# Kernel optimization log

Hardware: AMD Instinct MI355X
Metric: run time of the kernel (lower is better)

The kernel has to match this reference:

```python
import jax, jax.numpy as jnp
import numpy as np

M = 128      # grid length
J = 80       # number of functional features (hard-coded *80 in module)
NB = 2       # n_base (module-level global used in forward)
N = NB * J   # total tiny basis networks = 160
H = 256      # hidden width
B = 2048     # batch
LN_EPS = 1e-6


def _layernorm(z, alpha, beta):
    # torch LayerNorm variant: std is UNBIASED (torch.std default), eps added to std
    avg = z.mean(axis=-1, keepdims=True)
    std = jnp.sqrt(z.var(axis=-1, ddof=1, keepdims=True)) + LN_EPS
    return (z - avg) / std * alpha + beta


def setup_inputs() -> dict:
    key = jax.random.key(0)
    ks = jax.random.split(key, 10)
    bh = 1.0 / np.sqrt(H)  # torch Linear default init bound for fan_in=H
    u = lambda k, shp, b: jax.random.uniform(k, shp, jnp.float32, -b, b)
    return {
        "x": jax.random.normal(ks[0], (B, M, J), jnp.float32),
        "t": jnp.linspace(0.0, 1.0, M, dtype=jnp.float32),
        "W_in": u(ks[1], (N, 1, H), 1.0),        # fan_in = 1
        "b_in": u(ks[2], (N, H), 1.0),
        "W_h": u(ks[3], (3, N, H, H), bh),        # 3 hidden->hidden linears
        "b_h": u(ks[4], (3, N, H), bh),
        "W_out": u(ks[5], (N, H, 1), bh),
        "b_out": u(ks[6], (N, 1), bh),
        "ln_alpha": jax.random.normal(ks[7], (4, N, H), jnp.float32),
        "ln_beta": jax.random.normal(ks[8], (4, N, H), jnp.float32),
    }


def reference(x, t, W_in, b_in, W_h, b_h, W_out, b_out, ln_alpha, ln_beta):
    # --- evaluate all N tiny basis MLPs on the grid, batched ---
    # input layer: t (M,) x W_in (N,1,H) -> (N, M, H)
    z = jnp.einsum("m,nh->nmh", t, W_in[:, 0, :]) + b_in[:, None, :]
    z = z + _layernorm(z, ln_alpha[0][:, None, :], ln_beta[0][:, None, :])
    z = jax.nn.selu(z)  # dropout is identity in eval mode
    for i in range(3):
        z = jnp.einsum("nmh,nhk->nmk", z, W_h[i]) + b_h[i][:, None, :]
        z = z + _layernorm(z, ln_alpha[i + 1][:, None, :], ln_beta[i + 1][:, None, :])
        z = jax.nn.selu(z)
    bases = jnp.einsum("nmh,nh->nm", z, W_out[:, :, 0]) + b_out  # (N, M)

    # --- trapezoidal inner-product score ---
    h = t[1:] - t[:-1]                                   # (M-1,)
    w = jnp.zeros(M, x.dtype).at[:-1].add(h / 2).at[1:].add(h / 2)  # trapezoid weights
    bases_r = bases.reshape(J, NB, M)                    # basis i*NB+k serves feature i
    score = jnp.einsum("bmj,jkm,m->bjk", x, bases_r, w)  # (B, J, NB)
    return score.reshape(x.shape[0], J * NB)
```

## Files before the change

### kernel.cpp

```cpp
#include <hip/hip_runtime.h>
#include <math.h>

#define M_GRID 128
#define J_FEAT 80
#define NNET   160
#define HDIM   256

typedef __attribute__((ext_vector_type(8))) short v8s;
typedef __attribute__((ext_vector_type(4))) float f4;

__device__ __forceinline__ unsigned short f2bf(float f) {
    unsigned u = __float_as_uint(f);
    u += 0x7fffu + ((u >> 16) & 1u);
    return (unsigned short)(u >> 16);
}

__device__ __forceinline__ float selu_f(float x) {
    const float SC = 1.0507009873554805f;
    const float AL = 1.6732632423543772f;
    return x > 0.f ? SC * x : SC * AL * (__expf(x) - 1.f);
}

#define FENCE_BAR() do { asm volatile("s_waitcnt lgkmcnt(0)" ::: "memory"); \
                         __builtin_amdgcn_sched_barrier(0);                 \
                         __builtin_amdgcn_s_barrier(); } while (0)

__attribute__((amdgpu_flat_work_group_size(512, 512), amdgpu_waves_per_eu(2, 2)))
__global__ void basis_kernel(const float* __restrict__ t,
                             const float* __restrict__ W_in,
                             const float* __restrict__ b_in,
                             const float* __restrict__ W_h,
                             const float* __restrict__ b_h,
                             const float* __restrict__ W_out,
                             const float* __restrict__ b_out,
                             const float* __restrict__ ln_a,
                             const float* __restrict__ ln_b,
                             float* __restrict__ basesT)
{
    extern __shared__ __align__(16) unsigned char lds[];
    const int n    = blockIdx.x;
    const int tid  = threadIdx.x;
    const int l    = tid & 63;
    const int wv   = tid >> 6;
    const int lr   = l & 15;
    const int g    = l >> 4;
    const int jcol = tid & 255;
    const int o8   = tid >> 8;

    unsigned char* const actw = lds + 32768 + (size_t)wv * 8192;
    float* const P = (float*)(lds + 98304);

    float rr[2][16];
    auto issue = [&](float (&r)[16], int q) {
        const float* Wq = W_h + ((size_t)((q >> 3) * NNET + n) << 16)
                        + (size_t)((q & 7) * 32 + o8 * 16) * HDIM + jcol;
        #pragma unroll
        for (int i = 0; i < 16; ++i) r[i] = Wq[(size_t)i * HDIM];
    };
    auto convert_store = [&](float (&r)[16], int bufp) {
        #pragma unroll
        for (int o = 0; o < 2; ++o) {
            v8s pk;
            #pragma unroll
            for (int i = 0; i < 8; ++i) pk[i] = (short)f2bf(r[o * 8 + i]);
            int byte = (bufp << 14) + (o8 << 13) + jcol * 32 + (o << 4);
            byte ^= ((jcol >> 2) & 7) << 4;
            *(v8s*)(lds + byte) = pk;
        }
    };

    issue(rr[0], 0);
    issue(rr[1], 1);

    {
        const size_t nb = (size_t)n * HDIM;
        #pragma unroll
        for (int i = 0; i < 7; ++i) {
            const int idx = tid + (i << 9), grp = idx >> 8, off = idx & 255;
            float v;
            if (grp == 0)       v = W_out[nb + off];
            else if (grp < 4)   v = ln_a[((size_t)grp * NNET + n) * HDIM + off];
            else if (grp < 7)   v = ln_b[((size_t)(grp - 3) * NNET + n) * HDIM + off];
            else if (grp < 10)  v = b_h[((size_t)(grp - 7) * NNET + n) * HDIM + off];
            else if (grp == 10) v = W_in[nb + off];
            else if (grp == 11) v = b_in[nb + off];
            else if (grp == 12) v = ln_a[nb + off];
            else                v = ln_b[nb + off];
            P[idx] = v;
        }
    }
    FENCE_BAR();

    const float tval = t[wv * 16 + lr];
    {
        const float* wi = P + 2560; const float* bi = P + 2816;
        const float* la = P + 3072; const float* lb = P + 3328;
        float s_ = 0.f, q_ = 0.f;
        #pragma unroll
        for (int kt = 0; kt < 8; ++kt) {
            const int h0 = kt * 32 + g * 8;
            const f4 w0 = *(const f4*)(wi + h0), w1 = *(const f4*)(wi + h0 + 4);
            const f4 b0 = *(const f4*)(bi + h0), b1 = *(const f4*)(bi + h0 + 4);
            #pragma unroll
            for (int i = 0; i < 4; ++i) {
                float v0 = __builtin_fmaf(tval, w0[i], b0[i]);
                float v1 = __builtin_fmaf(tval, w1[i], b1[i]);
                s_ += v0 + v1; q_ += v0 * v0 + v1 * v1;
            }
        }
        s_ += __shfl_xor(s_, 16); q_ += __shfl_xor(q_, 16);
        s_ += __shfl_xor(s_, 32); q_ += __shfl_xor(q_, 32);
        const float mean = s_ * (1.f / 256.f);
        const float var  = (q_ - s_ * s_ * (1.f / 256.f)) * (1.f / 255.f);
        const float inv  = 1.f / (sqrtf(var) + 1e-6f);
        asm volatile("" ::: "memory");
        #pragma unroll
        for (int kt = 0; kt < 8; ++kt) {
            const int h0 = kt * 32 + g * 8;
            const f4 w0 = *(const f4*)(wi + h0), w1 = *(const f4*)(wi + h0 + 4);
            const f4 b0 = *(const f4*)(bi + h0), b1 = *(const f4*)(bi + h0 + 4);
            const f4 a0 = *(const f4*)(la + h0), a1 = *(const f4*)(la + h0 + 4);
            const f4 e0 = *(const f4*)(lb + h0), e1 = *(const f4*)(lb + h0 + 4);
            v8s a;
            #pragma unroll
            for (int i = 0; i < 4; ++i) {
                float v0 = __builtin_fmaf(tval, w0[i], b0[i]);
                float v1 = __builtin_fmaf(tval, w1[i], b1[i]);
                a[i]     = (short)f2bf(selu_f(v0 + (v0 - mean) * inv * a0[i] + e0[i]));
                a[i + 4] = (short)f2bf(selu_f(v1 + (v1 - mean) * inv * a1[i] + e1[i]));
            }
            *(v8s*)(actw + ((lr * 512 + h0 * 2) ^ (lr << 5))) = a;
        }
        asm volatile("s_waitcnt lgkmcnt(0)" ::: "memory");
    }

    f4 acc[16];

    #pragma unroll 1
    for (int L = 0; L < 3; ++L) {
        const f4 zero = {0.f, 0.f, 0.f, 0.f};
        #pragma unroll
        for (int ct = 0; ct < 16; ++ct) acc[ct] = zero;

        #pragma unroll
        for (int s = 0; s < 8; ++s) {
            const int q = L * 8 + s;
            convert_store(rr[s & 1], s & 1);
            if (q + 2 < 24) issue(rr[s & 1], q + 2);
            FENCE_BAR();
            const v8s af = *(const v8s*)(actw + ((lr * 512 + (s * 32 + g * 8) * 2) ^ (lr << 5)));
            #pragma unroll
            for (int ct = 0; ct < 16; ++ct) {
                const int jb = ct * 16 + lr;
                int byte = ((s & 1) << 14) + ((g >> 1) << 13) + jb * 32 + ((g & 1) << 4);
                byte ^= ((jb >> 2) & 7) << 4;
                const v8s bf = *(const v8s*)(lds + byte);
                acc[ct] = __builtin_amdgcn_mfma_f32_16x16x32_bf16(af, bf, acc[ct], 0, 0, 0);
            }
        }

        const float* bh = P + (7 + L) * 256;
        const float* la = P + (1 + L) * 256;
        const float* lb = P + (4 + L) * 256;

        float sums[4] = {0,0,0,0}, sqs[4] = {0,0,0,0};
        #pragma unroll
        for (int ct = 0; ct < 16; ++ct) {
            const float bias = bh[ct * 16 + lr];
            #pragma unroll
            for (int r = 0; r < 4; ++r) {
                float v = acc[ct][r] + bias;
                acc[ct][r] = v;
                sums[r] += v; sqs[r] += v * v;
            }
        }
        #pragma unroll
        for (int r = 0; r < 4; ++r)
            #pragma unroll
            for (int m = 1; m <= 8; m <<= 1) {
                sums[r] += __shfl_xor(sums[r], m);
                sqs[r]  += __shfl_xor(sqs[r],  m);
            }
        float mean[4], inv[4];
        #pragma unroll
        for (int r = 0; r < 4; ++r) {
            mean[r] = sums[r] * (1.f / 256.f);
            float var = (sqs[r] - sums[r] * sums[r] * (1.f / 256.f)) * (1.f / 255.f);
            inv[r] = 1.f / (sqrtf(var) + 1e-6f);
        }

        if (L < 2) {
            #pragma unroll
            for (int ct = 0; ct < 16; ++ct) {
                const float a_ = la[ct * 16 + lr], b_ = lb[ct * 16 + lr];
                #pragma unroll
                for (int r = 0; r < 4; ++r) {
                    float v  = acc[ct][r];
                    float sv = selu_f(v + (v - mean[r]) * inv[r] * a_ + b_);
                    const int row = 4 * g + r;
                    *(unsigned short*)(actw + ((row * 512 + (ct * 16 + lr) * 2) ^ (row << 5)))
                        = f2bf(sv);
                }
            }
            asm volatile("s_waitcnt lgkmcnt(0)" ::: "memory");
            __builtin_amdgcn_sched_barrier(0);
        } else {
            const float bo = b_out[n];
            float ps[4] = {0,0,0,0};
            #pragma unroll
            for (int ct = 0; ct < 16; ++ct) {
                const float a_ = la[ct * 16 + lr], b_ = lb[ct * 16 + lr];
                const float w_ = P[ct * 16 + lr];
                #pragma unroll
                for (int r = 0; r < 4; ++r) {
                    float v  = acc[ct][r];
                    float sv = selu_f(v + (v - mean[r]) * inv[r] * a_ + b_);
                    ps[r] += sv * w_;
                }
            }
            #pragma unroll
            for (int r = 0; r < 4; ++r)
                #pragma unroll
                for (int m = 1; m <= 8; m <<= 1)
                    ps[r] += __shfl_xor(ps[r], m);
            #pragma unroll
            for (int r = 0; r < 4; ++r)
                if (lr == r)
                    basesT[(size_t)(wv * 16 + 4 * g + r) * NNET + n] = ps[r] + bo;
        }
    }
}

__launch_bounds__(256)
__global__ void score_kernel(const float* __restrict__ x,
                             const float* __restrict__ t,
                             const float* __restrict__ basesT,
                             float* __restrict__ out)
{
    __shared__ float c_lds[M_GRID * 32];
    const int jt  = blockIdx.x;
    const int bt  = blockIdx.y;
    const int tid = threadIdx.x;

    for (int i = tid; i < M_GRID * 32; i += 256) {
        const int m  = i >> 5;
        const int jl = i & 31;
        const float tp = t[m == M_GRID - 1 ? M_GRID - 1 : m + 1];
        const float tm = t[m == 0 ? 0 : m - 1];
        c_lds[i] = basesT[(size_t)m * NNET + jt * 32 + jl] * 0.5f * (tp - tm);
    }
    __syncthreads();

    const int jj = tid & 31;
    const int bs = tid >> 5;
    const int jk = jt * 32 + jj;
    const int b  = bt * 8 + bs;
    const float* xp = x + (size_t)b * (M_GRID * J_FEAT) + (jk >> 1);
    float acc = 0.f;
    #pragma unroll 8
    for (int m = 0; m < M_GRID; ++m)
        acc += xp[(size_t)m * J_FEAT] * c_lds[m * 32 + jj];
    out[(size_t)b * NNET + jk] = acc;
}

extern "C" void kernel_launch(void* const* d_in, const int* in_sizes, int n_in,
                              void* d_out, int out_size, void* d_ws, size_t ws_size,
                              hipStream_t stream)
{
    const float* x     = (const float*)d_in[0];
    const float* t     = (const float*)d_in[1];
    const float* W_in  = (const float*)d_in[2];
    const float* b_in  = (const float*)d_in[3];
    const float* W_h   = (const float*)d_in[4];
    const float* b_h   = (const float*)d_in[5];
    const float* W_out = (const float*)d_in[6];
    const float* b_out = (const float*)d_in[7];
    const float* ln_a  = (const float*)d_in[8];
    const float* ln_b  = (const float*)d_in[9];
    float* basesT = (float*)d_ws;

    basis_kernel<<<dim3(NNET), dim3(512), 112640, stream>>>(
        t, W_in, b_in, W_h, b_h, W_out, b_out, ln_a, ln_b, basesT);
    score_kernel<<<dim3(5, 256), dim3(256), 0, stream>>>(
        x, t, basesT, (float*)d_out);
}
```

Before: 85.45 us.

## Specialize warps into weight-producer and MFMA-consumer groups in basis kernel

Doubles the basis kernel block to 1024 threads. Eight producer waves stream W_h slices from global memory, convert them to bf16 and store them into double-buffered LDS. Eight consumer waves only run the MFMA, layernorm and SELU epilogue, with one barrier per slice. The aim is to keep global load latency and conversion off the MFMA waves, at the cost of more threads and register pressure, and consumer waves idle while producers finish.

```diff
diff --git a/kernel.cpp b/kernel.cpp
--- a/kernel.cpp
+++ b/kernel.cpp
@@ -21,11 +21,10 @@
     return x > 0.f ? SC * x : SC * AL * (__expf(x) - 1.f);
 }
 
-#define FENCE_BAR() do { asm volatile("s_waitcnt lgkmcnt(0)" ::: "memory"); \
-                         __builtin_amdgcn_sched_barrier(0);                 \
-                         __builtin_amdgcn_s_barrier(); } while (0)
-
-__attribute__((amdgpu_flat_work_group_size(512, 512), amdgpu_waves_per_eu(2, 2)))
+#define RAW_BAR() do { __builtin_amdgcn_sched_barrier(0);                  \
+                       __builtin_amdgcn_s_barrier(); } while (0)
+
+__attribute__((amdgpu_flat_work_group_size(1024, 1024)))
 __global__ void basis_kernel(const float* __restrict__ t,
                              const float* __restrict__ W_in,
                              const float* __restrict__ b_in,
@@ -42,37 +41,37 @@
     const int tid  = threadIdx.x;
     const int l    = tid & 63;
     const int wv   = tid >> 6;
+    const bool cons = (wv < 8);
+    const int c    = wv & 7;
     const int lr   = l & 15;
     const int g    = l >> 4;
-    const int jcol = tid & 255;
-    const int o8   = tid >> 8;
-
-    unsigned char* const actw = lds + 32768 + (size_t)wv * 8192;
+    const int ptid = tid & 511;
+    const int jcol = ptid & 255;
+    const int o8   = ptid >> 8;
+
+    unsigned char* const actw = lds + 32768 + (size_t)c * 8192;
     float* const P = (float*)(lds + 98304);
 
-    float rr[2][16];
-    auto issue = [&](float (&r)[16], int q) {
+    float rr[16];
+    auto issue = [&](int q) {
         const float* Wq = W_h + ((size_t)((q >> 3) * NNET + n) << 16)
                         + (size_t)((q & 7) * 32 + o8 * 16) * HDIM + jcol;
         #pragma unroll
-        for (int i = 0; i < 16; ++i) r[i] = Wq[(size_t)i * HDIM];
+        for (int i = 0; i < 16; ++i) rr[i] = Wq[(size_t)i * HDIM];
     };
-    auto convert_store = [&](float (&r)[16], int bufp) {
+    auto convert_store = [&](int bufp) {
         #pragma unroll
         for (int o = 0; o < 2; ++o) {
             v8s pk;
             #pragma unroll
-            for (int i = 0; i < 8; ++i) pk[i] = (short)f2bf(r[o * 8 + i]);
+            for (int i = 0; i < 8; ++i) pk[i] = (short)f2bf(rr[o * 8 + i]);
             int byte = (bufp << 14) + (o8 << 13) + jcol * 32 + (o << 4);
             byte ^= ((jcol >> 2) & 7) << 4;
             *(v8s*)(lds + byte) = pk;
         }
     };
 
-    issue(rr[0], 0);
-    issue(rr[1], 1);
-
-    {
+    if (cons) {
         const size_t nb = (size_t)n * HDIM;
         #pragma unroll
         for (int i = 0; i < 7; ++i) {
@@ -88,11 +87,14 @@
             else                v = ln_b[nb + off];
             P[idx] = v;
         }
+        asm volatile("s_waitcnt lgkmcnt(0)" ::: "memory");
+    } else {
+        issue(0);
     }
-    FENCE_BAR();
-
-    const float tval = t[wv * 16 + lr];
-    {
+    RAW_BAR();
+
+    if (cons) {
+        const float tval = t[c * 16 + lr];
         const float* wi = P + 2560; const float* bi = P + 2816;
         const float* la = P + 3072; const float* lb = P + 3328;
         float s_ = 0.f, q_ = 0.f;
@@ -132,102 +134,114 @@
             *(v8s*)(actw + ((lr * 512 + h0 * 2) ^ (lr << 5))) = a;
         }
         asm volatile("s_waitcnt lgkmcnt(0)" ::: "memory");
+    } else {
+        convert_store(0);
+        asm volatile("s_waitcnt lgkmcnt(0)" ::: "memory");
+        issue(1);
     }
+    RAW_BAR();
 
     f4 acc[16];
 
     #pragma unroll 1
-    for (int L = 0; L < 3; ++L) {
-        const f4 zero = {0.f, 0.f, 0.f, 0.f};
-        #pragma unroll
-        for (int ct = 0; ct < 16; ++ct) acc[ct] = zero;
-
-        #pragma unroll
-        for (int s = 0; s < 8; ++s) {
-            const int q = L * 8 + s;
-            convert_store(rr[s & 1], s & 1);
-            if (q + 2 < 24) issue(rr[s & 1], q + 2);
-            FENCE_BAR();
+    for (int q = 0; q < 24; ++q) {
+        if (cons) {
+            const int s = q & 7, L = q >> 3;
+            if (s == 0) {
+                const f4 zero = {0.f, 0.f, 0.f, 0.f};
+                #pragma unroll
+                for (int ct = 0; ct < 16; ++ct) acc[ct] = zero;
+            }
             const v8s af = *(const v8s*)(actw + ((lr * 512 + (s * 32 + g * 8) * 2) ^ (lr << 5)));
             #pragma unroll
-            for (int ct = 0; ct < 16; ++ct) {
-                const int jb = ct * 16 + lr;
-                int byte = ((s & 1) << 14) + ((g >> 1) << 13) + jb * 32 + ((g & 1) << 4);
-                byte ^= ((jb >> 2) & 7) << 4;
-                const v8s bf = *(const v8s*)(lds + byte);
-                acc[ct] = __builtin_amdgcn_mfma_f32_16x16x32_bf16(af, bf, acc[ct], 0, 0, 0);
-            }
-        }
-
-        const float* bh = P + (7 + L) * 256;
-        const float* la = P + (1 + L) * 256;
-        const float* lb = P + (4 + L) * 256;
-
-        float sums[4] = {0,0,0,0}, sqs[4] = {0,0,0,0};
-        #pragma unroll
-        for (int ct = 0; ct < 16; ++ct) {
-            const float bias = bh[ct * 16 + lr];
-            #pragma unroll
-            for (int r = 0; r < 4; ++r) {
-                float v = acc[ct][r] + bias;
-                acc[ct][r] = v;
-                sums[r] += v; sqs[r] += v * v;
-            }
-        }
-        #pragma unroll
-        for (int r = 0; r < 4; ++r)
-            #pragma unroll
-            for (int m = 1; m <= 8; m <<= 1) {
-                sums[r] += __shfl_xor(sums[r], m);
-                sqs[r]  += __shfl_xor(sqs[r],  m);
-            }
-        float mean[4], inv[4];
-        #pragma unroll
-        for (int r = 0; r < 4; ++r) {
-            mean[r] = sums[r] * (1.f / 256.f);
-            float var = (sqs[r] - sums[r] * sums[r] * (1.f / 256.f)) * (1.f / 255.f);
-            inv[r] = 1.f / (sqrtf(var) + 1e-6f);
-        }
-
-        if (L < 2) {
-            #pragma unroll
-            for (int ct = 0; ct < 16; ++ct) {
-                const float a_ = la[ct * 16 + lr], b_ = lb[ct * 16 + lr];
+            for (int cc = 0; cc < 4; ++cc) {
+                #pragma unroll
+                for (int c4 = 0; c4 < 4; ++c4) {
+                    const int ct = cc * 4 + c4;
+                    const int jb = ct * 16 + lr;
+                    int byte = ((q & 1) << 14) + ((g >> 1) << 13) + jb * 32 + ((g & 1) << 4);
+                    byte ^= ((jb >> 2) & 7) << 4;
+                    const v8s bf = *(const v8s*)(lds + byte);
+                    acc[ct] = __builtin_amdgcn_mfma_f32_16x16x32_bf16(af, bf, acc[ct], 0, 0, 0);
+                }
+                __builtin_amdgcn_sched_barrier(0);
+            }
+            if (s == 7) {
+                const float* bh = P + (7 + L) * 256;
+                const float* la = P + (1 + L) * 256;
+                const float* lb = P + (4 + L) * 256;
+                float sums[4] = {0,0,0,0}, sqs[4] = {0,0,0,0};
+                #pragma unroll
+                for (int ct = 0; ct < 16; ++ct) {
+                    const float bias = bh[ct * 16 + lr];
+                    #pragma unroll
+                    for (int r = 0; r < 4; ++r) {
+                        float v = acc[ct][r] + bias;
+                        acc[ct][r] = v;
+                        sums[r] += v; sqs[r] += v * v;
+                    }
+                }
+                #pragma unroll
+                for (int r = 0; r < 4; ++r)
+                    #pragma unroll
+                    for (int m = 1; m <= 8; m <<= 1) {
+                        sums[r] += __shfl_xor(sums[r], m);
+                        sqs[r]  += __shfl_xor(sqs[r],  m);
+                    }
+                float mean[4], inv[4];
                 #pragma unroll
                 for (int r = 0; r < 4; ++r) {
-                    float v  = acc[ct][r];
-                    float sv = selu_f(v + (v - mean[r]) * inv[r] * a_ + b_);
-                    const int row = 4 * g + r;
-                    *(unsigned short*)(actw + ((row * 512 + (ct * 16 + lr) * 2) ^ (row << 5)))
-                        = f2bf(sv);
+                    mean[r] = sums[r] * (1.f / 256.f);
+                    float var = (sqs[r] - sums[r] * sums[r] * (1.f / 256.f)) * (1.f / 255.f);
+                    inv[r] = 1.f / (sqrtf(var) + 1e-6f);
                 }
-            }
-            asm volatile("s_waitcnt lgkmcnt(0)" ::: "memory");
-            __builtin_amdgcn_sched_barrier(0);
+                if (L < 2) {
+                    #pragma unroll
+                    for (int ct = 0; ct < 16; ++ct) {
+                        const float a_ = la[ct * 16 + lr], b_ = lb[ct * 16 + lr];
+                        #pragma unroll
+                        for (int r = 0; r < 4; ++r) {
+                            float v  = acc[ct][r];
+                            float sv = selu_f(v + (v - mean[r]) * inv[r] * a_ + b_);
+                            const int row = 4 * g + r;
+                            *(unsigned short*)(actw + ((row * 512 + (ct * 16 + lr) * 2) ^ (row << 5)))
+                                = f2bf(sv);
+                        }
+                    }
+                    asm volatile("s_waitcnt lgkmcnt(0)" ::: "memory");
+                } else {
+                    const float bo = b_out[n];
+                    float ps[4] = {0,0,0,0};
+                    #pragma unroll
+                    for (int ct = 0; ct < 16; ++ct) {
+                        const float a_ = la[ct * 16 + lr], b_ = lb[ct * 16 + lr];
+                        const float w_ = P[ct * 16 + lr];
+                        #pragma unroll
+                        for (int r = 0; r < 4; ++r) {
+                            float v  = acc[ct][r];
+                            float sv = selu_f(v + (v - mean[r]) * inv[r] * a_ + b_);
+                            ps[r] += sv * w_;
+                        }
+                    }
+                    #pragma unroll
+                    for (int r = 0; r < 4; ++r)
+                        #pragma unroll
+                        for (int m = 1; m <= 8; m <<= 1)
+                            ps[r] += __shfl_xor(ps[r], m);
+                    #pragma unroll
+                    for (int r = 0; r < 4; ++r)
+                        if (lr == r)
+                            basesT[(size_t)(c * 16 + 4 * g + r) * NNET + n] = ps[r] + bo;
+                }
+            }
         } else {
-            const float bo = b_out[n];
-            float ps[4] = {0,0,0,0};
-            #pragma unroll
-            for (int ct = 0; ct < 16; ++ct) {
-                const float a_ = la[ct * 16 + lr], b_ = lb[ct * 16 + lr];
-                const float w_ = P[ct * 16 + lr];
-                #pragma unroll
-                for (int r = 0; r < 4; ++r) {
-                    float v  = acc[ct][r];
-                    float sv = selu_f(v + (v - mean[r]) * inv[r] * a_ + b_);
-                    ps[r] += sv * w_;
-                }
-            }
-            #pragma unroll
-            for (int r = 0; r < 4; ++r)
-                #pragma unroll
-                for (int m = 1; m <= 8; m <<= 1)
-                    ps[r] += __shfl_xor(ps[r], m);
-            #pragma unroll
-            for (int r = 0; r < 4; ++r)
-                if (lr == r)
-                    basesT[(size_t)(wv * 16 + 4 * g + r) * NNET + n] = ps[r] + bo;
-        }
+            if (q + 1 < 24) {
+                convert_store((q + 1) & 1);
+                asm volatile("s_waitcnt lgkmcnt(0)" ::: "memory");
+                if (q + 2 < 24) issue(q + 2);
+            }
+        }
+        RAW_BAR();
     }
 }
 
@@ -279,7 +293,7 @@
     const float* ln_b  = (const float*)d_in[9];
     float* basesT = (float*)d_ws;
 
-    basis_kernel<<<dim3(NNET), dim3(512), 112640, stream>>>(
+    basis_kernel<<<dim3(NNET), dim3(1024), 112640, stream>>>(
         t, W_in, b_in, W_h, b_h, W_out, b_out, ln_a, ln_b, basesT);
     score_kernel<<<dim3(5, 256), dim3(256), 0, stream>>>(
         x, t, basesT, (float*)d_out);
```

Result: slower. 277.4 us (+224.6%).

## Halve basis block to 4 waves, each computing 32 rows with overlapped weight staging

Applied to the files above, without the earlier changes.

Shrinks the basis kernel from 512 to 256 threads, so each wave now handles two 16-row tiles. Each B fragment read from LDS feeds two MFMAs, which halves LDS traffic per MFMA. The weight pipeline is restructured so the bf16 conversion and store of the next K-slice, plus its global prefetch, are interleaved with the MFMAs of the current slice, with one barrier per slice. This costs more registers (two 32-float prefetch buffers and two accumulator sets) and fewer waves to hide latency.

```diff
diff --git a/kernel.cpp b/kernel.cpp
--- a/kernel.cpp
+++ b/kernel.cpp
@@ -25,7 +25,7 @@
                          __builtin_amdgcn_sched_barrier(0);                 \
                          __builtin_amdgcn_s_barrier(); } while (0)
 
-__attribute__((amdgpu_flat_work_group_size(512, 512), amdgpu_waves_per_eu(2, 2)))
+__attribute__((amdgpu_flat_work_group_size(256, 256), amdgpu_waves_per_eu(1, 1)))
 __global__ void basis_kernel(const float* __restrict__ t,
                              const float* __restrict__ W_in,
                              const float* __restrict__ b_in,
@@ -44,189 +44,232 @@
     const int wv   = tid >> 6;
     const int lr   = l & 15;
     const int g    = l >> 4;
-    const int jcol = tid & 255;
-    const int o8   = tid >> 8;
-
-    unsigned char* const actw = lds + 32768 + (size_t)wv * 8192;
+    const int jcol = tid;
+
+    unsigned char* const actw = lds + 32768 + (size_t)wv * 16384;
     float* const P = (float*)(lds + 98304);
 
-    float rr[2][16];
-    auto issue = [&](float (&r)[16], int q) {
+    float rrA[32], rrB[32];
+    auto issueA = [&](int q) {
         const float* Wq = W_h + ((size_t)((q >> 3) * NNET + n) << 16)
-                        + (size_t)((q & 7) * 32 + o8 * 16) * HDIM + jcol;
-        #pragma unroll
-        for (int i = 0; i < 16; ++i) r[i] = Wq[(size_t)i * HDIM];
-    };
-    auto convert_store = [&](float (&r)[16], int bufp) {
-        #pragma unroll
-        for (int o = 0; o < 2; ++o) {
+                        + (size_t)((q & 7) * 32) * HDIM + jcol;
+        #pragma unroll
+        for (int i = 0; i < 32; ++i) rrA[i] = Wq[(size_t)i * HDIM];
+    };
+    auto issueB = [&](int q) {
+        const float* Wq = W_h + ((size_t)((q >> 3) * NNET + n) << 16)
+                        + (size_t)((q & 7) * 32) * HDIM + jcol;
+        #pragma unroll
+        for (int i = 0; i < 32; ++i) rrB[i] = Wq[(size_t)i * HDIM];
+    };
+    auto convA = [&](int bufp) {
+        #pragma unroll
+        for (int o = 0; o < 4; ++o) {
             v8s pk;
             #pragma unroll
-            for (int i = 0; i < 8; ++i) pk[i] = (short)f2bf(r[o * 8 + i]);
-            int byte = (bufp << 14) + (o8 << 13) + jcol * 32 + (o << 4);
+            for (int i = 0; i < 8; ++i) pk[i] = (short)f2bf(rrA[o * 8 + i]);
+            int byte = (bufp << 14) + ((o >> 1) << 13) + jcol * 32 + ((o & 1) << 4);
             byte ^= ((jcol >> 2) & 7) << 4;
             *(v8s*)(lds + byte) = pk;
         }
     };
-
-    issue(rr[0], 0);
-    issue(rr[1], 1);
+    auto convB = [&](int bufp) {
+        #pragma unroll
+        for (int o = 0; o < 4; ++o) {
+            v8s pk;
+            #pragma unroll
+            for (int i = 0; i < 8; ++i) pk[i] = (short)f2bf(rrB[o * 8 + i]);
+            int byte = (bufp << 14) + ((o >> 1) << 13) + jcol * 32 + ((o & 1) << 4);
+            byte ^= ((jcol >> 2) & 7) << 4;
+            *(v8s*)(lds + byte) = pk;
+        }
+    };
+
+    issueA(0);
+    issueB(1);
 
     {
         const size_t nb = (size_t)n * HDIM;
         #pragma unroll
-        for (int i = 0; i < 7; ++i) {
-            const int idx = tid + (i << 9), grp = idx >> 8, off = idx & 255;
+        for (int grp = 0; grp < 14; ++grp) {
             float v;
-            if (grp == 0)       v = W_out[nb + off];
-            else if (grp < 4)   v = ln_a[((size_t)grp * NNET + n) * HDIM + off];
-            else if (grp < 7)   v = ln_b[((size_t)(grp - 3) * NNET + n) * HDIM + off];
-            else if (grp < 10)  v = b_h[((size_t)(grp - 7) * NNET + n) * HDIM + off];
-            else if (grp == 10) v = W_in[nb + off];
-            else if (grp == 11) v = b_in[nb + off];
-            else if (grp == 12) v = ln_a[nb + off];
-            else                v = ln_b[nb + off];
-            P[idx] = v;
+            if (grp == 0)       v = W_out[nb + tid];
+            else if (grp < 4)   v = ln_a[((size_t)grp * NNET + n) * HDIM + tid];
+            else if (grp < 7)   v = ln_b[((size_t)(grp - 3) * NNET + n) * HDIM + tid];
+            else if (grp < 10)  v = b_h[((size_t)(grp - 7) * NNET + n) * HDIM + tid];
+            else if (grp == 10) v = W_in[nb + tid];
+            else if (grp == 11) v = b_in[nb + tid];
+            else if (grp == 12) v = ln_a[nb + tid];
+            else                v = ln_b[nb + tid];
+            P[grp * 256 + tid] = v;
         }
     }
     FENCE_BAR();
 
-    const float tval = t[wv * 16 + lr];
     {
         const float* wi = P + 2560; const float* bi = P + 2816;
         const float* la = P + 3072; const float* lb = P + 3328;
-        float s_ = 0.f, q_ = 0.f;
-        #pragma unroll
-        for (int kt = 0; kt < 8; ++kt) {
-            const int h0 = kt * 32 + g * 8;
-            const f4 w0 = *(const f4*)(wi + h0), w1 = *(const f4*)(wi + h0 + 4);
-            const f4 b0 = *(const f4*)(bi + h0), b1 = *(const f4*)(bi + h0 + 4);
-            #pragma unroll
-            for (int i = 0; i < 4; ++i) {
-                float v0 = __builtin_fmaf(tval, w0[i], b0[i]);
-                float v1 = __builtin_fmaf(tval, w1[i], b1[i]);
-                s_ += v0 + v1; q_ += v0 * v0 + v1 * v1;
-            }
-        }
-        s_ += __shfl_xor(s_, 16); q_ += __shfl_xor(q_, 16);
-        s_ += __shfl_xor(s_, 32); q_ += __shfl_xor(q_, 32);
-        const float mean = s_ * (1.f / 256.f);
-        const float var  = (q_ - s_ * s_ * (1.f / 256.f)) * (1.f / 255.f);
-        const float inv  = 1.f / (sqrtf(var) + 1e-6f);
-        asm volatile("" ::: "memory");
-        #pragma unroll
-        for (int kt = 0; kt < 8; ++kt) {
-            const int h0 = kt * 32 + g * 8;
-            const f4 w0 = *(const f4*)(wi + h0), w1 = *(const f4*)(wi + h0 + 4);
-            const f4 b0 = *(const f4*)(bi + h0), b1 = *(const f4*)(bi + h0 + 4);
-            const f4 a0 = *(const f4*)(la + h0), a1 = *(const f4*)(la + h0 + 4);
-            const f4 e0 = *(const f4*)(lb + h0), e1 = *(const f4*)(lb + h0 + 4);
-            v8s a;
-            #pragma unroll
-            for (int i = 0; i < 4; ++i) {
-                float v0 = __builtin_fmaf(tval, w0[i], b0[i]);
-                float v1 = __builtin_fmaf(tval, w1[i], b1[i]);
-                a[i]     = (short)f2bf(selu_f(v0 + (v0 - mean) * inv * a0[i] + e0[i]));
-                a[i + 4] = (short)f2bf(selu_f(v1 + (v1 - mean) * inv * a1[i] + e1[i]));
-            }
-            *(v8s*)(actw + ((lr * 512 + h0 * 2) ^ (lr << 5))) = a;
+        #pragma unroll
+        for (int tt = 0; tt < 2; ++tt) {
+            const float tval = t[wv * 32 + tt * 16 + lr];
+            float s_ = 0.f, q_ = 0.f;
+            #pragma unroll
+            for (int kt = 0; kt < 8; ++kt) {
+                const int h0 = kt * 32 + g * 8;
+                const f4 w0 = *(const f4*)(wi + h0), w1 = *(const f4*)(wi + h0 + 4);
+                const f4 b0 = *(const f4*)(bi + h0), b1 = *(const f4*)(bi + h0 + 4);
+                #pragma unroll
+                for (int i = 0; i < 4; ++i) {
+                    float v0 = __builtin_fmaf(tval, w0[i], b0[i]);
+                    float v1 = __builtin_fmaf(tval, w1[i], b1[i]);
+                    s_ += v0 + v1; q_ += v0 * v0 + v1 * v1;
+                }
+            }
+            s_ += __shfl_xor(s_, 16); q_ += __shfl_xor(q_, 16);
+            s_ += __shfl_xor(s_, 32); q_ += __shfl_xor(q_, 32);
+            const float mean = s_ * (1.f / 256.f);
+            const float var  = (q_ - s_ * s_ * (1.f / 256.f)) * (1.f / 255.f);
+            const float inv  = 1.f / (sqrtf(var) + 1e-6f);
+            asm volatile("" ::: "memory");
+            #pragma unroll
+            for (int kt = 0; kt < 8; ++kt) {
+                const int h0 = kt * 32 + g * 8;
+                const f4 w0 = *(const f4*)(wi + h0), w1 = *(const f4*)(wi + h0 + 4);
+                const f4 b0 = *(const f4*)(bi + h0), b1 = *(const f4*)(bi + h0 + 4);
+                const f4 a0 = *(const f4*)(la + h0), a1 = *(const f4*)(la + h0 + 4);
+                const f4 e0 = *(const f4*)(lb + h0), e1 = *(const f4*)(lb + h0 + 4);
+                v8s a;
+                #pragma unroll
+                for (int i = 0; i < 4; ++i) {
+                    float v0 = __builtin_fmaf(tval, w0[i], b0[i]);
+                    float v1 = __builtin_fmaf(tval, w1[i], b1[i]);
+                    a[i]     = (short)f2bf(selu_f(v0 + (v0 - mean) * inv * a0[i] + e0[i]));
+                    a[i + 4] = (short)f2bf(selu_f(v1 + (v1 - mean) * inv * a1[i] + e1[i]));
+                }
+                *(v8s*)(actw + tt * 8192 + ((lr * 512 + h0 * 2) ^ (lr << 5))) = a;
+            }
+            asm volatile("" ::: "memory");
         }
         asm volatile("s_waitcnt lgkmcnt(0)" ::: "memory");
     }
 
-    f4 acc[16];
-
-    #pragma unroll 1
-    for (int L = 0; L < 3; ++L) {
-        const f4 zero = {0.f, 0.f, 0.f, 0.f};
-        #pragma unroll
-        for (int ct = 0; ct < 16; ++ct) acc[ct] = zero;
-
-        #pragma unroll
-        for (int s = 0; s < 8; ++s) {
-            const int q = L * 8 + s;
-            convert_store(rr[s & 1], s & 1);
-            if (q + 2 < 24) issue(rr[s & 1], q + 2);
-            FENCE_BAR();
-            const v8s af = *(const v8s*)(actw + ((lr * 512 + (s * 32 + g * 8) * 2) ^ (lr << 5)));
-            #pragma unroll
-            for (int ct = 0; ct < 16; ++ct) {
-                const int jb = ct * 16 + lr;
-                int byte = ((s & 1) << 14) + ((g >> 1) << 13) + jb * 32 + ((g & 1) << 4);
-                byte ^= ((jb >> 2) & 7) << 4;
-                const v8s bf = *(const v8s*)(lds + byte);
-                acc[ct] = __builtin_amdgcn_mfma_f32_16x16x32_bf16(af, bf, acc[ct], 0, 0, 0);
-            }
-        }
-
+    convA(0);
+    issueA(2);
+    FENCE_BAR();
+
+    f4 acc[2][16];
+
+    auto mfma_body = [&](int q, int tb) {
+        const int sq = q & 7;
+        const v8s afA = *(const v8s*)(actw + ((lr * 512 + (sq * 32 + g * 8) * 2) ^ (lr << 5)));
+        const v8s afB = *(const v8s*)(actw + 8192 + ((lr * 512 + (sq * 32 + g * 8) * 2) ^ (lr << 5)));
+        #pragma unroll
+        for (int ct = 0; ct < 16; ++ct) {
+            const int jb = ct * 16 + lr;
+            int byte = (tb << 14) + ((g >> 1) << 13) + jb * 32 + ((g & 1) << 4);
+            byte ^= ((jb >> 2) & 7) << 4;
+            const v8s bf = *(const v8s*)(lds + byte);
+            acc[0][ct] = __builtin_amdgcn_mfma_f32_16x16x32_bf16(afA, bf, acc[0][ct], 0, 0, 0);
+            acc[1][ct] = __builtin_amdgcn_mfma_f32_16x16x32_bf16(afB, bf, acc[1][ct], 0, 0, 0);
+        }
+    };
+    auto epilogue = [&](int L) {
         const float* bh = P + (7 + L) * 256;
         const float* la = P + (1 + L) * 256;
         const float* lb = P + (4 + L) * 256;
-
-        float sums[4] = {0,0,0,0}, sqs[4] = {0,0,0,0};
-        #pragma unroll
-        for (int ct = 0; ct < 16; ++ct) {
-            const float bias = bh[ct * 16 + lr];
+        #pragma unroll
+        for (int tt = 0; tt < 2; ++tt) {
+            float sums[4] = {0,0,0,0}, sqs[4] = {0,0,0,0};
+            #pragma unroll
+            for (int ct = 0; ct < 16; ++ct) {
+                const float bias = bh[ct * 16 + lr];
+                #pragma unroll
+                for (int r = 0; r < 4; ++r) {
+                    float v = acc[tt][ct][r] + bias;
+                    acc[tt][ct][r] = v;
+                    sums[r] += v; sqs[r] += v * v;
+                }
+            }
+            #pragma unroll
+            for (int r = 0; r < 4; ++r)
+                #pragma unroll
+                for (int m = 1; m <= 8; m <<= 1) {
+                    sums[r] += __shfl_xor(sums[r], m);
+                    sqs[r]  += __shfl_xor(sqs[r],  m);
+                }
+            float mean[4], inv[4];
             #pragma unroll
             for (int r = 0; r < 4; ++r) {
-                float v = acc[ct][r] + bias;
-                acc[ct][r] = v;
-                sums[r] += v; sqs[r] += v * v;
-            }
-        }
-        #pragma unroll
-        for (int r = 0; r < 4; ++r)
-            #pragma unroll
-            for (int m = 1; m <= 8; m <<= 1) {
-                sums[r] += __shfl_xor(sums[r], m);
-                sqs[r]  += __shfl_xor(sqs[r],  m);
-            }
-        float mean[4], inv[4];
-        #pragma unroll
-        for (int r = 0; r < 4; ++r) {
-            mean[r] = sums[r] * (1.f / 256.f);
-            float var = (sqs[r] - sums[r] * sums[r] * (1.f / 256.f)) * (1.f / 255.f);
-            inv[r] = 1.f / (sqrtf(var) + 1e-6f);
-        }
-
-        if (L < 2) {
-            #pragma unroll
-            for (int ct = 0; ct < 16; ++ct) {
-                const float a_ = la[ct * 16 + lr], b_ = lb[ct * 16 + lr];
-                #pragma unroll
-                for (int r = 0; r < 4; ++r) {
-                    float v  = acc[ct][r];
-                    float sv = selu_f(v + (v - mean[r]) * inv[r] * a_ + b_);
-                    const int row = 4 * g + r;
-                    *(unsigned short*)(actw + ((row * 512 + (ct * 16 + lr) * 2) ^ (row << 5)))
-                        = f2bf(sv);
-                }
-            }
-            asm volatile("s_waitcnt lgkmcnt(0)" ::: "memory");
-            __builtin_amdgcn_sched_barrier(0);
-        } else {
-            const float bo = b_out[n];
-            float ps[4] = {0,0,0,0};
-            #pragma unroll
-            for (int ct = 0; ct < 16; ++ct) {
-                const float a_ = la[ct * 16 + lr], b_ = lb[ct * 16 + lr];
-                const float w_ = P[ct * 16 + lr];
-                #pragma unroll
-                for (int r = 0; r < 4; ++r) {
-                    float v  = acc[ct][r];
-                    float sv = selu_f(v + (v - mean[r]) * inv[r] * a_ + b_);
-                    ps[r] += sv * w_;
-                }
-            }
-            #pragma unroll
-            for (int r = 0; r < 4; ++r)
-                #pragma unroll
-                for (int m = 1; m <= 8; m <<= 1)
-                    ps[r] += __shfl_xor(ps[r], m);
-            #pragma unroll
-            for (int r = 0; r < 4; ++r)
-                if (lr == r)
-                    basesT[(size_t)(wv * 16 + 4 * g + r) * NNET + n] = ps[r] + bo;
+                mean[r] = sums[r] * (1.f / 256.f);
+                float var = (sqs[r] - sums[r] * sums[r] * (1.f / 256.f)) * (1.f / 255.f);
+                inv[r] = 1.f / (sqrtf(var) + 1e-6f);
+            }
+            if (L < 2) {
+                #pragma unroll
+                for (int ct = 0; ct < 16; ++ct) {
+                    const float a_ = la[ct * 16 + lr], b_ = lb[ct * 16 + lr];
+                    #pragma unroll
+                    for (int r = 0; r < 4; ++r) {
+                        float v  = acc[tt][ct][r];
+                        float sv = selu_f(v + (v - mean[r]) * inv[r] * a_ + b_);
+                        const int row = 4 * g + r;
+                        *(unsigned short*)(actw + tt * 8192
+                            + ((row * 512 + (ct * 16 + lr) * 2) ^ (row << 5))) = f2bf(sv);
+                    }
+                }
+            } else {
+                const float bo = b_out[n];
+                float ps[4] = {0,0,0,0};
+                #pragma unroll
+                for (int ct = 0; ct < 16; ++ct) {
+                    const float a_ = la[ct * 16 + lr], b_ = lb[ct * 16 + lr];
+                    const float w_ = P[ct * 16 + lr];
+                    #pragma unroll
+                    for (int r = 0; r < 4; ++r) {
+                        float v  = acc[tt][ct][r];
+                        float sv = selu_f(v + (v - mean[r]) * inv[r] * a_ + b_);
+                        ps[r] += sv * w_;
+                    }
+                }
+                #pragma unroll
+                for (int r = 0; r < 4; ++r)
+                    #pragma unroll
+                    for (int m = 1; m <= 8; m <<= 1)
+                        ps[r] += __shfl_xor(ps[r], m);
+                #pragma unroll
+                for (int r = 0; r < 4; ++r)
+                    if (lr == r)
+                        basesT[(size_t)(wv * 32 + tt * 16 + 4 * g + r) * NNET + n] = ps[r] + bo;
+            }
+        }
+        asm volatile("s_waitcnt lgkmcnt(0)" ::: "memory");
+    };
+
+    #pragma unroll 1
+    for (int p = 0; p < 12; ++p) {
+        {
+            const int q = 2 * p;
+            if ((q & 7) == 0) {
+                const f4 zero = {0.f, 0.f, 0.f, 0.f};
+                #pragma unroll
+                for (int tt = 0; tt < 2; ++tt)
+                    #pragma unroll
+                    for (int ct = 0; ct < 16; ++ct) acc[tt][ct] = zero;
+            }
+            convB(1);
+            if (2 * p + 3 < 24) issueB(2 * p + 3);
+            mfma_body(q, 0);
+            FENCE_BAR();
+        }
+        {
+            const int q = 2 * p + 1;
+            if (2 * p + 2 < 24) {
+                convA(0);
+                if (2 * p + 4 < 24) issueA(2 * p + 4);
+            }
+            mfma_body(q, 1);
+            if ((q & 7) == 7) epilogue(q >> 3);
+            if (p < 11) FENCE_BAR();
         }
     }
 }
@@ -279,7 +322,7 @@
     const float* ln_b  = (const float*)d_in[9];
     float* basesT = (float*)d_ws;
 
-    basis_kernel<<<dim3(NNET), dim3(512), 112640, stream>>>(
+    basis_kernel<<<dim3(NNET), dim3(256), 112640, stream>>>(
         t, W_in, b_in, W_h, b_h, W_out, b_out, ln_a, ln_b, basesT);
     score_kernel<<<dim3(5, 256), dim3(256), 0, stream>>>(
         x, t, basesT, (float*)d_out);
```

Result: slower. 123.1 us (+44.1%).
